# Optimization experiments

Hardware: AMD Instinct MI355X
Metric: run time of the kernel (lower is better)

## Reference

```python
import jax, jax.numpy as jnp
import numpy as np
from functools import partial


def _gcn_norm(edge_index, n):
    # PyG gcn_norm with add_self_loops=True, edge_weight=1.
    src, dst = edge_index[0], edge_index[1]
    loop = jnp.arange(n, dtype=src.dtype)
    src = jnp.concatenate([src, loop])
    dst = jnp.concatenate([dst, loop])
    deg = jax.ops.segment_sum(jnp.ones_like(dst, dtype=jnp.float32), dst, num_segments=n)
    dinv = jnp.where(deg > 0, jax.lax.rsqrt(deg), 0.0)
    norm = dinv[src] * dinv[dst]  # [E+N]
    return src, dst, norm


def _gcn_conv(x, W, b, src, dst, norm, n):
    h = x @ W                                   # [N, out]
    msg = h[src] * norm[:, None]                # [E+N, out] gather + scale
    out = jax.ops.segment_sum(msg, dst, num_segments=n)  # scatter-add
    return out + b


def setup_inputs() -> dict:
    key = jax.random.key(0)
    ks = jax.random.split(key, 8)
    N, E, IN, OUT = 100000, 1600000, 128, 32
    H = 2 * OUT
    def glorot(k, shape):
        lim = float(np.sqrt(6.0 / (shape[0] + shape[1])))
        return jax.random.uniform(k, shape, jnp.float32, -lim, lim)
    return {
        "x": jax.random.normal(ks[0], (N, IN), jnp.float32),
        "edge_index": jax.random.randint(ks[1], (2, E), 0, N, jnp.int64),
        "W1": glorot(ks[2], (IN, H)),
        "b1": jnp.zeros((H,), jnp.float32),
        "W_mu": glorot(ks[3], (H, OUT)),
        "b_mu": jnp.zeros((OUT,), jnp.float32),
        "W_log": glorot(ks[4], (H, OUT)),
        "b_log": jnp.zeros((OUT,), jnp.float32),
    }


def reference(x, edge_index, W1, b1, W_mu, b_mu, W_log, b_log):
    n = x.shape[0]
    src, dst, norm = _gcn_norm(edge_index, n)
    h = _gcn_conv(x, W1, b1, src, dst, norm, n)
    h = jax.nn.relu(h)
    mu = _gcn_conv(h, W_mu, b_mu, src, dst, norm, n)
    log = _gcn_conv(h, W_log, b_log, src, dst, norm, n)
    return (mu, log)
```

## Files before the change

### kernel.cpp

```cpp
#include <hip/hip_runtime.h>
#include <hip/hip_fp16.h>


#define EPB 8192

__device__ inline uint2 f4_to_h4(float4 v) {
    __half2 lo = __floats2half2_rn(v.x, v.y);
    __half2 hi = __floats2half2_rn(v.z, v.w);
    uint2 u;
    u.x = *reinterpret_cast<unsigned int*>(&lo);
    u.y = *reinterpret_cast<unsigned int*>(&hi);
    return u;
}
__device__ inline float4 h4_to_f4(uint2 u) {
    __half2 lo = *reinterpret_cast<__half2*>(&u.x);
    __half2 hi = *reinterpret_cast<__half2*>(&u.y);
    float2 a = __half22float2(lo);
    float2 b = __half22float2(hi);
    return make_float4(a.x, a.y, b.x, b.y);
}

__global__ __launch_bounds__(256) void k_fused1(const int* __restrict__ ei, int E,
                                                int* __restrict__ hist, int NB, int shift,
                                                const float* __restrict__ x,
                                                const float* __restrict__ W1,
                                                __half* __restrict__ A, int N, int NEB) {
    __shared__ float Ws[8192];
    int t = threadIdx.x;
    int b = blockIdx.x;
    if (b < NEB) {
        int* h = (int*)Ws;
        for (int k = t; k < NB; k += 256) h[k] = 0;
        __syncthreads();
        int e0 = b * EPB, e1 = min(e0 + EPB, E);
        for (int e = e0 + t * 4; e < e1; e += 1024) {
            if (e + 3 < e1 && ((E & 3) == 0)) {
                int4 d4 = *reinterpret_cast<const int4*>(ei + E + e);
                atomicAdd(&h[d4.x >> shift], 1);
                atomicAdd(&h[d4.y >> shift], 1);
                atomicAdd(&h[d4.z >> shift], 1);
                atomicAdd(&h[d4.w >> shift], 1);
            } else {
                for (int k2 = 0; k2 < 4; ++k2) {
                    int e2 = e + k2;
                    if (e2 < e1) atomicAdd(&h[ei[E + e2] >> shift], 1);
                }
            }
        }
        __syncthreads();
        for (int k = t; k < NB; k += 256) hist[(size_t)b * NB + k] = h[k];
        return;
    }
    int bb = b - NEB;
    for (int i = t; i < 2048; i += 256)
        reinterpret_cast<float4*>(Ws)[i] = reinterpret_cast<const float4*>(W1)[i];
    __syncthreads();
    int cg = t & 15, rg = t >> 4;
    int row0 = bb * 128 + rg * 8;
    int c4 = cg * 4;
    float4 acc[8];
#pragma unroll
    for (int i = 0; i < 8; ++i) acc[i] = {0.f, 0.f, 0.f, 0.f};
    for (int k0 = 0; k0 < 128; k0 += 4) {
        float4 xr[8];
#pragma unroll
        for (int i = 0; i < 8; ++i) {
            int rr = row0 + i;
            if (rr >= N) rr = N - 1;
            xr[i] = *reinterpret_cast<const float4*>(x + (size_t)rr * 128 + k0);
        }
#pragma unroll
        for (int kk = 0; kk < 4; ++kk) {
            float4 w = *reinterpret_cast<const float4*>(Ws + (k0 + kk) * 64 + c4);
#pragma unroll
            for (int i = 0; i < 8; ++i) {
                float xv = (&xr[i].x)[kk];
                acc[i].x = fmaf(xv, w.x, acc[i].x);
                acc[i].y = fmaf(xv, w.y, acc[i].y);
                acc[i].z = fmaf(xv, w.z, acc[i].z);
                acc[i].w = fmaf(xv, w.w, acc[i].w);
            }
        }
    }
#pragma unroll
    for (int i = 0; i < 8; ++i) {
        int rr = row0 + i;
        if (rr < N)
            *reinterpret_cast<uint2*>(A + (size_t)rr * 64 + c4) = f4_to_h4(acc[i]);
    }
}

__global__ void k_colpre(int* __restrict__ hist, int* __restrict__ colTotal,
                         int NB, int NBLK) {
    int k = blockIdx.x * 256 + threadIdx.x;
    if (k >= NB) return;
    int run = 0;
#pragma unroll 4
    for (int b = 0; b < NBLK; ++b) {
        int* p = hist + (size_t)b * NB + k;
        int v = *p;
        *p = run;
        run += v;
    }
    colTotal[k] = run;
}

__global__ __launch_bounds__(256) void k_bscan(const int* __restrict__ colTotal,
                                               int* __restrict__ bucketStart,
                                               int NB, int E,
                                               int* __restrict__ rowptr, int N) {
    __shared__ int sdata[256];
    int t = threadIdx.x;
    int v[8];
    int sum = 0;
#pragma unroll
    for (int i = 0; i < 8; ++i) {
        int k = t * 8 + i;
        v[i] = (k < NB) ? colTotal[k] : 0;
        sum += v[i];
    }
    sdata[t] = sum;
    __syncthreads();
    for (int off = 1; off < 256; off <<= 1) {
        int val = (t >= off) ? sdata[t - off] : 0;
        __syncthreads();
        sdata[t] += val;
        __syncthreads();
    }
    int excl = (t > 0) ? sdata[t - 1] : 0;
#pragma unroll
    for (int i = 0; i < 8; ++i) {
        int k = t * 8 + i;
        if (k < NB) bucketStart[k] = excl;
        excl += v[i];
    }
    if (t == 0) { bucketStart[NB] = E; rowptr[N] = E; }
}

__global__ __launch_bounds__(256) void k_part(const int* __restrict__ ei, int E,
                                              const int* __restrict__ hist,
                                              const int* __restrict__ bucketStart,
                                              int NB, int shift,
                                              int2* __restrict__ part) {
    __shared__ int cur[2048];
    int t = threadIdx.x, b = blockIdx.x;
    for (int k = t; k < NB; k += 256)
        cur[k] = hist[(size_t)b * NB + k] + bucketStart[k];
    __syncthreads();
    int e0 = b * EPB, e1 = min(e0 + EPB, E);
    for (int e = e0 + t * 4; e < e1; e += 1024) {
        if (e + 3 < e1 && ((E & 3) == 0)) {
            int4 s4 = *reinterpret_cast<const int4*>(ei + e);
            int4 d4 = *reinterpret_cast<const int4*>(ei + E + e);
            int p;
            p = atomicAdd(&cur[d4.x >> shift], 1); part[p] = make_int2(s4.x, d4.x);
            p = atomicAdd(&cur[d4.y >> shift], 1); part[p] = make_int2(s4.y, d4.y);
            p = atomicAdd(&cur[d4.z >> shift], 1); part[p] = make_int2(s4.z, d4.z);
            p = atomicAdd(&cur[d4.w >> shift], 1); part[p] = make_int2(s4.w, d4.w);
        } else {
            for (int k2 = 0; k2 < 4; ++k2) {
                int e2 = e + k2;
                if (e2 < e1) {
                    int s = ei[e2], d = ei[E + e2];
                    int p = atomicAdd(&cur[d >> shift], 1);
                    part[p] = make_int2(s, d);
                }
            }
        }
    }
}

__global__ __launch_bounds__(256) void k_bucket(const int2* __restrict__ part,
                                                const int* __restrict__ bucketStart,
                                                int NB, int shift,
                                                int* __restrict__ ssrc,
                                                int* __restrict__ rowptr,
                                                float* __restrict__ dinv, int N) {
    __shared__ int cnt[2048];
    __shared__ int base[2048];
    int t = threadIdx.x, b = blockIdx.x;
    int lo = bucketStart[b], hi = bucketStart[b + 1];
    int n0 = b << shift;
    int nn = min(1 << shift, N - n0);
    for (int i = t; i < nn; i += 256) cnt[i] = 0;
    __syncthreads();
    for (int e = lo + t; e < hi; e += 256) {
        int2 pd = part[e];
        atomicAdd(&cnt[pd.y - n0], 1);
    }
    __syncthreads();
    if (t == 0) {
        int run = 0;
        for (int i = 0; i < nn; ++i) { base[i] = run; run += cnt[i]; }
    }
    __syncthreads();
    for (int i = t; i < nn; i += 256) {
        rowptr[n0 + i] = lo + base[i];
        dinv[n0 + i] = rsqrtf((float)(cnt[i] + 1));
    }
    __syncthreads();
    for (int e = lo + t; e < hi; e += 256) {
        int2 pd = part[e];
        int p = atomicAdd(&base[pd.y - n0], 1);
        ssrc[lo + p] = pd.x;
    }
}

template <int EPI>
__global__ __launch_bounds__(256) void k_agg(const int* __restrict__ rowptr,
                                             const int* __restrict__ ssrc,
                                             const float* __restrict__ dinv,
                                             const __half* __restrict__ feat,
                                             const float* __restrict__ bias,
                                             __half* __restrict__ out, int N) {
    int idx = blockIdx.x * 256 + threadIdx.x;
    int g = idx >> 4;
    if (g >= N) return;
    int fo = idx & 15;
    const uint2* F = reinterpret_cast<const uint2*>(feat);
    int beg = rowptr[g], end = rowptr[g + 1];
    float dd = dinv[g];
    float4 self = h4_to_f4(F[(size_t)g * 16 + fo]);
    float4 a0, a1 = {0,0,0,0}, a2 = {0,0,0,0}, a3 = {0,0,0,0};
    if (EPI == 1) { a0.x = self.x * dd; a0.y = self.y * dd; a0.z = self.z * dd; a0.w = self.w * dd; }
    else a0 = self;
    int j = beg;
    for (; j + 4 <= end; j += 4) {
        int s0 = ssrc[j], s1 = ssrc[j + 1], s2 = ssrc[j + 2], s3 = ssrc[j + 3];
        float4 v0 = h4_to_f4(F[(size_t)s0 * 16 + fo]);
        float4 v1 = h4_to_f4(F[(size_t)s1 * 16 + fo]);
        float4 v2 = h4_to_f4(F[(size_t)s2 * 16 + fo]);
        float4 v3 = h4_to_f4(F[(size_t)s3 * 16 + fo]);
        if (EPI == 1) {
            float n0 = dinv[s0], n1 = dinv[s1], n2 = dinv[s2], n3 = dinv[s3];
            a0.x = fmaf(v0.x, n0, a0.x); a0.y = fmaf(v0.y, n0, a0.y);
            a0.z = fmaf(v0.z, n0, a0.z); a0.w = fmaf(v0.w, n0, a0.w);
            a1.x = fmaf(v1.x, n1, a1.x); a1.y = fmaf(v1.y, n1, a1.y);
            a1.z = fmaf(v1.z, n1, a1.z); a1.w = fmaf(v1.w, n1, a1.w);
            a2.x = fmaf(v2.x, n2, a2.x); a2.y = fmaf(v2.y, n2, a2.y);
            a2.z = fmaf(v2.z, n2, a2.z); a2.w = fmaf(v2.w, n2, a2.w);
            a3.x = fmaf(v3.x, n3, a3.x); a3.y = fmaf(v3.y, n3, a3.y);
            a3.z = fmaf(v3.z, n3, a3.z); a3.w = fmaf(v3.w, n3, a3.w);
        } else {
            a0.x += v0.x; a0.y += v0.y; a0.z += v0.z; a0.w += v0.w;
            a1.x += v1.x; a1.y += v1.y; a1.z += v1.z; a1.w += v1.w;
            a2.x += v2.x; a2.y += v2.y; a2.z += v2.z; a2.w += v2.w;
            a3.x += v3.x; a3.y += v3.y; a3.z += v3.z; a3.w += v3.w;
        }
    }
    for (; j < end; ++j) {
        int s = ssrc[j];
        float4 v = h4_to_f4(F[(size_t)s * 16 + fo]);
        if (EPI == 1) {
            float ns = dinv[s];
            a1.x = fmaf(v.x, ns, a1.x); a1.y = fmaf(v.y, ns, a1.y);
            a1.z = fmaf(v.z, ns, a1.z); a1.w = fmaf(v.w, ns, a1.w);
        } else {
            a1.x += v.x; a1.y += v.y; a1.z += v.z; a1.w += v.w;
        }
    }
    float4 acc;
    acc.x = (a0.x + a1.x) + (a2.x + a3.x);
    acc.y = (a0.y + a1.y) + (a2.y + a3.y);
    acc.z = (a0.z + a1.z) + (a2.z + a3.z);
    acc.w = (a0.w + a1.w) + (a2.w + a3.w);
    float4 r;
    if (EPI == 1) {
        const float4 bv = *reinterpret_cast<const float4*>(bias + (fo << 2));
        r.x = fmaf(acc.x, dd, bv.x);
        r.y = fmaf(acc.y, dd, bv.y);
        r.z = fmaf(acc.z, dd, bv.z);
        r.w = fmaf(acc.w, dd, bv.w);
        r.x = r.x > 0.f ? r.x * dd : 0.f;
        r.y = r.y > 0.f ? r.y * dd : 0.f;
        r.z = r.z > 0.f ? r.z * dd : 0.f;
        r.w = r.w > 0.f ? r.w * dd : 0.f;
    } else {
        r.x = acc.x * dd; r.y = acc.y * dd; r.z = acc.z * dd; r.w = acc.w * dd;
    }
    reinterpret_cast<uint2*>(out)[(size_t)g * 16 + fo] = f4_to_h4(r);
}

__global__ __launch_bounds__(256) void k_final2(const __half* __restrict__ R,
                                                const float* __restrict__ Wmu,
                                                const float* __restrict__ bmu,
                                                const float* __restrict__ Wlg,
                                                const float* __restrict__ blg,
                                                float* __restrict__ out, int N) {
    __shared__ float Ws[64 * 64];
    int t = threadIdx.x;
    for (int i = t; i < 4096; i += 256) {
        int k = i >> 6, c = i & 63;
        Ws[i] = (c < 32) ? Wmu[(k << 5) + c] : Wlg[(k << 5) + (c - 32)];
    }
    __syncthreads();
    int cg = t & 15, rg = t >> 4;
    int row0 = blockIdx.x * 128 + rg * 8;
    int c4 = cg * 4;
    float4 bv;
    if (c4 < 32) bv = *reinterpret_cast<const float4*>(bmu + c4);
    else         bv = *reinterpret_cast<const float4*>(blg + c4 - 32);
    float4 acc[8];
#pragma unroll
    for (int i = 0; i < 8; ++i) acc[i] = bv;
    const uint2* R2 = reinterpret_cast<const uint2*>(R);
    for (int k0 = 0; k0 < 64; k0 += 4) {
        float4 xr[8];
#pragma unroll
        for (int i = 0; i < 8; ++i) {
            int rr = row0 + i;
            if (rr >= N) rr = N - 1;
            xr[i] = h4_to_f4(R2[(size_t)rr * 16 + (k0 >> 2)]);
        }
#pragma unroll
        for (int kk = 0; kk < 4; ++kk) {
            float4 w = *reinterpret_cast<const float4*>(Ws + (k0 + kk) * 64 + c4);
#pragma unroll
            for (int i = 0; i < 8; ++i) {
                float xv = (&xr[i].x)[kk];
                acc[i].x = fmaf(xv, w.x, acc[i].x);
                acc[i].y = fmaf(xv, w.y, acc[i].y);
                acc[i].z = fmaf(xv, w.z, acc[i].z);
                acc[i].w = fmaf(xv, w.w, acc[i].w);
            }
        }
    }
#pragma unroll
    for (int i = 0; i < 8; ++i) {
        int rr = row0 + i;
        if (rr < N) {
            float* dst = (c4 < 32) ? (out + (size_t)rr * 32 + c4)
                                   : (out + (size_t)N * 32 + (size_t)rr * 32 + (c4 - 32));
            *reinterpret_cast<float4*>(dst) = acc[i];
        }
    }
}

extern "C" void kernel_launch(void* const* d_in, const int* in_sizes, int n_in,
                              void* d_out, int out_size, void* d_ws, size_t ws_size,
                              hipStream_t stream) {
    const float* x   = (const float*)d_in[0];
    const int*   ei  = (const int*)d_in[1];
    const float* W1  = (const float*)d_in[2];
    const float* b1  = (const float*)d_in[3];
    const float* Wmu = (const float*)d_in[4];
    const float* bmu = (const float*)d_in[5];
    const float* Wlg = (const float*)d_in[6];
    const float* blg = (const float*)d_in[7];
    float* out = (float*)d_out;

    const int N = in_sizes[0] / 128;
    const int E = in_sizes[1] / 2;

    int shift = 6;
    while ((((N + (1 << shift) - 1) >> shift)) > 2048) ++shift;
    const int NB  = (N + (1 << shift) - 1) >> shift;
    const int NEB = (E + EPB - 1) / EPB;
    const int GB  = (N + 127) / 128;
    const int AB  = (int)(((size_t)N * 16 + 255) / 256);

    __half* Ah        = (__half*)d_ws;
    __half* Bh        = Ah + (size_t)N * 64;
    int*    ssrc      = (int*)(Bh + (size_t)N * 64);
    int*    rowptr    = ssrc + E;
    float*  dinv      = (float*)(rowptr + (N + 1));
    int2*   part      = (int2*)(dinv + N);
    int*    hist      = (int*)(part + E);
    int*    colTotal  = hist + (size_t)NEB * NB;
    int*    bucketStart = colTotal + NB;

    k_fused1<<<NEB + GB, 256, 0, stream>>>(ei, E, hist, NB, shift, x, W1, Ah, N, NEB);
    k_colpre<<<(NB + 255) / 256, 256, 0, stream>>>(hist, colTotal, NB, NEB);
    k_bscan<<<1, 256, 0, stream>>>(colTotal, bucketStart, NB, E, rowptr, N);
    k_part<<<NEB, 256, 0, stream>>>(ei, E, hist, bucketStart, NB, shift, part);
    k_bucket<<<NB, 256, 0, stream>>>(part, bucketStart, NB, shift, ssrc, rowptr, dinv, N);

    k_agg<1><<<AB, 256, 0, stream>>>(rowptr, ssrc, dinv, Ah, b1, Bh, N);
    k_agg<2><<<AB, 256, 0, stream>>>(rowptr, ssrc, dinv, Bh, b1, Ah, N);

    k_final2<<<GB, 256, 0, stream>>>(Ah, Wmu, bmu, Wlg, blg, out, N);
}
```

Baseline: 295.8 us.

## Stage x tiles through shared memory and pack partition entries into 32 bits

The first-layer GEMM now loads 128x16 chunks of x cooperatively into LDS with coalesced float4 loads, and threads read their rows from LDS. Before, each thread made strided per-row global reads. Separately, the edge partition buffer now stores one 32-bit word per edge (source shifted left, low bits of destination) instead of an int2. This halves the scatter writes in k_part and the two reads in k_bucket. The packing assumes source index << shift fits in 32 bits, and the GEMM adds extra barriers per chunk.

Measured after the change: 284.6 us. 3.8% less time.

```diff
diff --git a/kernel.cpp b/kernel.cpp
--- a/kernel.cpp
+++ b/kernel.cpp
@@ -26,6 +26,7 @@
                                                 const float* __restrict__ W1,
                                                 __half* __restrict__ A, int N, int NEB) {
     __shared__ float Ws[8192];
+    __shared__ float xs[128 * 16];
     int t = threadIdx.x;
     int b = blockIdx.x;
     if (b < NEB) {
@@ -54,31 +55,44 @@
     int bb = b - NEB;
     for (int i = t; i < 2048; i += 256)
         reinterpret_cast<float4*>(Ws)[i] = reinterpret_cast<const float4*>(W1)[i];
-    __syncthreads();
     int cg = t & 15, rg = t >> 4;
-    int row0 = bb * 128 + rg * 8;
+    int rowB = bb * 128;
+    int row0 = rowB + rg * 8;
     int c4 = cg * 4;
     float4 acc[8];
 #pragma unroll
     for (int i = 0; i < 8; ++i) acc[i] = {0.f, 0.f, 0.f, 0.f};
-    for (int k0 = 0; k0 < 128; k0 += 4) {
-        float4 xr[8];
-#pragma unroll
-        for (int i = 0; i < 8; ++i) {
-            int rr = row0 + i;
-            if (rr >= N) rr = N - 1;
-            xr[i] = *reinterpret_cast<const float4*>(x + (size_t)rr * 128 + k0);
-        }
-#pragma unroll
-        for (int kk = 0; kk < 4; ++kk) {
-            float4 w = *reinterpret_cast<const float4*>(Ws + (k0 + kk) * 64 + c4);
-#pragma unroll
-            for (int i = 0; i < 8; ++i) {
-                float xv = (&xr[i].x)[kk];
-                acc[i].x = fmaf(xv, w.x, acc[i].x);
-                acc[i].y = fmaf(xv, w.y, acc[i].y);
-                acc[i].z = fmaf(xv, w.z, acc[i].z);
-                acc[i].w = fmaf(xv, w.w, acc[i].w);
+    for (int kc = 0; kc < 128; kc += 16) {
+        __syncthreads();
+#pragma unroll
+        for (int q = 0; q < 2; ++q) {
+            int slot = q * 256 + t;
+            int row = slot >> 2;
+            int f4 = (slot & 3) << 2;
+            int rr = rowB + row;
+            float4 v = {0.f, 0.f, 0.f, 0.f};
+            if (rr < N)
+                v = *reinterpret_cast<const float4*>(x + (size_t)rr * 128 + kc + f4);
+            *reinterpret_cast<float4*>(xs + row * 16 + f4) = v;
+        }
+        __syncthreads();
+#pragma unroll
+        for (int kk0 = 0; kk0 < 16; kk0 += 4) {
+            float4 xr[8];
+#pragma unroll
+            for (int i = 0; i < 8; ++i)
+                xr[i] = *reinterpret_cast<const float4*>(xs + (rg * 8 + i) * 16 + kk0);
+#pragma unroll
+            for (int kk = 0; kk < 4; ++kk) {
+                float4 w = *reinterpret_cast<const float4*>(Ws + (kc + kk0 + kk) * 64 + c4);
+#pragma unroll
+                for (int i = 0; i < 8; ++i) {
+                    float xv = (&xr[i].x)[kk];
+                    acc[i].x = fmaf(xv, w.x, acc[i].x);
+                    acc[i].y = fmaf(xv, w.y, acc[i].y);
+                    acc[i].z = fmaf(xv, w.z, acc[i].z);
+                    acc[i].w = fmaf(xv, w.w, acc[i].w);
+                }
             }
         }
     }
@@ -141,9 +155,10 @@
                                               const int* __restrict__ hist,
                                               const int* __restrict__ bucketStart,
                                               int NB, int shift,
-                                              int2* __restrict__ part) {
+                                              unsigned int* __restrict__ part) {
     __shared__ int cur[2048];
     int t = threadIdx.x, b = blockIdx.x;
+    unsigned int mask = (1u << shift) - 1u;
     for (int k = t; k < NB; k += 256)
         cur[k] = hist[(size_t)b * NB + k] + bucketStart[k];
     __syncthreads();
@@ -153,24 +168,28 @@
             int4 s4 = *reinterpret_cast<const int4*>(ei + e);
             int4 d4 = *reinterpret_cast<const int4*>(ei + E + e);
             int p;
-            p = atomicAdd(&cur[d4.x >> shift], 1); part[p] = make_int2(s4.x, d4.x);
-            p = atomicAdd(&cur[d4.y >> shift], 1); part[p] = make_int2(s4.y, d4.y);
-            p = atomicAdd(&cur[d4.z >> shift], 1); part[p] = make_int2(s4.z, d4.z);
-            p = atomicAdd(&cur[d4.w >> shift], 1); part[p] = make_int2(s4.w, d4.w);
+            p = atomicAdd(&cur[d4.x >> shift], 1);
+            part[p] = ((unsigned int)s4.x << shift) | ((unsigned int)d4.x & mask);
+            p = atomicAdd(&cur[d4.y >> shift], 1);
+            part[p] = ((unsigned int)s4.y << shift) | ((unsigned int)d4.y & mask);
+            p = atomicAdd(&cur[d4.z >> shift], 1);
+            part[p] = ((unsigned int)s4.z << shift) | ((unsigned int)d4.z & mask);
+            p = atomicAdd(&cur[d4.w >> shift], 1);
+            part[p] = ((unsigned int)s4.w << shift) | ((unsigned int)d4.w & mask);
         } else {
             for (int k2 = 0; k2 < 4; ++k2) {
                 int e2 = e + k2;
                 if (e2 < e1) {
                     int s = ei[e2], d = ei[E + e2];
                     int p = atomicAdd(&cur[d >> shift], 1);
-                    part[p] = make_int2(s, d);
+                    part[p] = ((unsigned int)s << shift) | ((unsigned int)d & mask);
                 }
             }
         }
     }
 }
 
-__global__ __launch_bounds__(256) void k_bucket(const int2* __restrict__ part,
+__global__ __launch_bounds__(256) void k_bucket(const unsigned int* __restrict__ part,
                                                 const int* __restrict__ bucketStart,
                                                 int NB, int shift,
                                                 int* __restrict__ ssrc,
@@ -179,14 +198,15 @@
     __shared__ int cnt[2048];
     __shared__ int base[2048];
     int t = threadIdx.x, b = blockIdx.x;
+    unsigned int mask = (1u << shift) - 1u;
     int lo = bucketStart[b], hi = bucketStart[b + 1];
     int n0 = b << shift;
     int nn = min(1 << shift, N - n0);
     for (int i = t; i < nn; i += 256) cnt[i] = 0;
     __syncthreads();
     for (int e = lo + t; e < hi; e += 256) {
-        int2 pd = part[e];
-        atomicAdd(&cnt[pd.y - n0], 1);
+        unsigned int pv = part[e];
+        atomicAdd(&cnt[pv & mask], 1);
     }
     __syncthreads();
     if (t == 0) {
@@ -200,9 +220,9 @@
     }
     __syncthreads();
     for (int e = lo + t; e < hi; e += 256) {
-        int2 pd = part[e];
-        int p = atomicAdd(&base[pd.y - n0], 1);
-        ssrc[lo + p] = pd.x;
+        unsigned int pv = part[e];
+        int p = atomicAdd(&base[pv & mask], 1);
+        ssrc[lo + p] = (int)(pv >> shift);
     }
 }
 
@@ -364,7 +384,7 @@
     int*    ssrc      = (int*)(Bh + (size_t)N * 64);
     int*    rowptr    = ssrc + E;
     float*  dinv      = (float*)(rowptr + (N + 1));
-    int2*   part      = (int2*)(dinv + N);
+    unsigned int* part = (unsigned int*)(dinv + N);
     int*    hist      = (int*)(part + E);
     int*    colTotal  = hist + (size_t)NEB * NB;
     int*    bucketStart = colTotal + NB;
```
